# Kernel optimization log

Measured on AMD Instinct MI355X. Metric: run time of the kernel, lower is better.

The kernel has to match this reference:

```python
import jax, jax.numpy as jnp
import numpy as np

M_B, M_S, D_IN, D_OUT = 4, 2048, 4096, 4096
SPARSITY_KEEP = 0.1


def setup_inputs() -> dict:
    key = jax.random.key(0)
    k1, k2, k3, k4 = jax.random.split(key, 4)
    data = jax.random.normal(k1, (M_B, M_S, D_IN), dtype=jnp.float32)
    weight = jax.random.normal(k2, (D_OUT, D_IN), dtype=jnp.float32) * 0.02
    w_mask = (jax.random.uniform(k3, (D_OUT, D_IN)) < SPARSITY_KEEP).astype(jnp.float32)
    bias_p = jax.random.normal(k4, (D_OUT,), dtype=jnp.float32) * 0.02
    return {"data": data, "weight": weight, "w_mask": w_mask, "bias_p": bias_p}


def reference(data, weight, w_mask, bias_p):
    # Equivalent math to CSR-conversion + sparse GEMM: out = data @ (W*mask)^T + b
    w = weight * w_mask                      # [D_OUT, D_IN]
    out = jnp.einsum('bsk,nk->bsn', data, w)  # [B, S, D_OUT]
    return out + bias_p
```

## Files before the change

### kernel.cpp

```cpp
#include <hip/hip_runtime.h>
#include <hip/hip_bf16.h>


#define M_TOT 8192
#define N_TOT 4096
#define K_TOT 4096

#define BM 256
#define BN 256
#define BK 64
#define NT (K_TOT / BK)

typedef __attribute__((ext_vector_type(8))) short short8;
typedef __attribute__((ext_vector_type(4))) float floatx4;

__device__ inline unsigned short f2bf(float f) {
    unsigned int u = __builtin_bit_cast(unsigned int, f);
    u += 0x7fffu + ((u >> 16) & 1u);
    return (unsigned short)(u >> 16);
}

__global__ __launch_bounds__(256) void cast_data_kernel(const float4* __restrict__ in,
                                                        ushort4* __restrict__ out) {
    int i = blockIdx.x * 256 + threadIdx.x;
    float4 f = in[i];
    ushort4 o;
    o.x = f2bf(f.x); o.y = f2bf(f.y); o.z = f2bf(f.z); o.w = f2bf(f.w);
    out[i] = o;
}

__global__ __launch_bounds__(256) void cast_w_kernel(const float4* __restrict__ w,
                                                     const float4* __restrict__ m,
                                                     ushort4* __restrict__ out) {
    int i = blockIdx.x * 256 + threadIdx.x;
    float4 a = w[i];
    float4 b = m[i];
    ushort4 o;
    o.x = f2bf(a.x * b.x); o.y = f2bf(a.y * b.y);
    o.z = f2bf(a.z * b.z); o.w = f2bf(a.w * b.w);
    out[i] = o;
}

__device__ inline void load_lds16(const unsigned short* g, unsigned short* l) {
    __builtin_amdgcn_global_load_lds(
        (__attribute__((address_space(1))) void*)(const_cast<unsigned short*>(g)),
        (__attribute__((address_space(3))) void*)(l),
        16, 0, 0);
}

#define BAR()   __builtin_amdgcn_s_barrier()
#define SB0()   __builtin_amdgcn_sched_barrier(0)
#define LGKM0() do { asm volatile("s_waitcnt lgkmcnt(0)" ::: "memory"); SB0(); } while (0)
#define VM8()   asm volatile("s_waitcnt vmcnt(8)" ::: "memory")
#define VM0()   asm volatile("s_waitcnt vmcnt(0)" ::: "memory")

__global__ __launch_bounds__(512, 2) void gemm_bt_kernel(const unsigned short* __restrict__ A,
                                                         const unsigned short* __restrict__ W,
                                                         const float* __restrict__ bias,
                                                         float* __restrict__ out) {
    __shared__ __align__(16) unsigned short As[2 * BM * BK];
    __shared__ __align__(16) unsigned short Bs[2 * BN * BK];

    const int t = threadIdx.x;
    const int m0 = blockIdx.y * BM;
    const int n0 = blockIdx.x * BN;

    const int lane  = t & 63;
    const int wv    = t >> 6;
    const int wm    = (wv >> 2) * 128;
    const int wn    = (wv & 3) * 64;
    const int row16 = lane & 15;
    const int quad  = lane >> 4;
    const int rx    = row16 & 7;

    const int srow  = t >> 3;
    const int lslot = (t & 7) ^ (srow & 7);
    const size_t thr_off = (size_t)srow * K_TOT + (size_t)lslot * 8;

    const unsigned short* Ag = A + (size_t)m0 * K_TOT + thr_off;
    const unsigned short* Bg = W + (size_t)n0 * K_TOT + thr_off;

    auto stageA = [&](int ts, int h) {
        const unsigned short* s = Ag + (size_t)(h * 128) * K_TOT + ts * BK;
        unsigned short* d = As + (ts & 1) * (BM * BK) + h * (128 * BK) + t * 8;
        load_lds16(s, d);
        load_lds16(s + (size_t)64 * K_TOT, d + 512 * 8);
    };
    auto stageB = [&](int ts, int h) {
        const unsigned short* s = Bg + (size_t)(h * 128) * K_TOT + ts * BK;
        unsigned short* d = Bs + (ts & 1) * (BN * BK) + h * (128 * BK) + t * 8;
        load_lds16(s, d);
        load_lds16(s + (size_t)64 * K_TOT, d + 512 * 8);
    };

    short8 af[4][2];
    short8 bf[2][2][2];

    auto readA_half = [&](int buf, int mh) {
#pragma unroll
        for (int i = 0; i < 4; i++) {
            const unsigned short* base =
                As + buf * (BM * BK) + (wm + mh * 64 + i * 16 + row16) * BK;
            af[i][0] = *(const short8*)(base + ((quad ^ rx) << 3));
            af[i][1] = *(const short8*)(base + (((4 + quad) ^ rx) << 3));
        }
    };
    auto readB_all = [&](int buf) {
#pragma unroll
        for (int nh = 0; nh < 2; nh++)
#pragma unroll
            for (int j = 0; j < 2; j++) {
                const unsigned short* base =
                    Bs + buf * (BN * BK) + (wn + nh * 32 + j * 16 + row16) * BK;
                bf[nh][j][0] = *(const short8*)(base + ((quad ^ rx) << 3));
                bf[nh][j][1] = *(const short8*)(base + (((4 + quad) ^ rx) << 3));
            }
    };

    floatx4 acc[8][4];
#pragma unroll
    for (int i = 0; i < 8; i++)
#pragma unroll
        for (int j = 0; j < 4; j++) {
            floatx4 z = {0.0f, 0.0f, 0.0f, 0.0f};
            acc[i][j] = z;
        }

    auto mmaQ = [&](int mh, int nh) {
        __builtin_amdgcn_s_setprio(1);
#pragma unroll
        for (int i = 0; i < 4; i++)
#pragma unroll
            for (int j = 0; j < 2; j++)
#pragma unroll
                for (int ks = 0; ks < 2; ks++)
                    acc[mh * 4 + i][nh * 2 + j] = __builtin_amdgcn_mfma_f32_16x16x32_bf16(
                        af[i][ks], bf[nh][j][ks], acc[mh * 4 + i][nh * 2 + j], 0, 0, 0);
        __builtin_amdgcn_s_setprio(0);
    };

    auto tile = [&](int kt, int mode) {
        const int buf = kt & 1;
        readA_half(buf, 0);
        readB_all(buf);
        BAR(); LGKM0();
        mmaQ(0, 0);
        BAR();
        if (mode == 0) stageB(kt + 2, 0);
        BAR(); SB0();
        mmaQ(0, 1);
        BAR();
        readA_half(buf, 1);
        if (mode == 0) stageB(kt + 2, 1);
        BAR(); LGKM0();
        mmaQ(1, 1);
        BAR();
        if (mode == 0) { stageA(kt + 2, 0); stageA(kt + 2, 1); VM8(); }
        if (mode == 1) { VM0(); }
        BAR(); SB0();
        mmaQ(1, 0);
        if (mode != 2) BAR();
    };

    stageB(0, 0); stageB(0, 1); stageA(0, 0); stageA(0, 1);
    stageB(1, 0); stageB(1, 1); stageA(1, 0); stageA(1, 1);
    VM8();
    BAR();

    for (int kt = 0; kt < NT - 2; ++kt)
        tile(kt, 0);
    tile(NT - 2, 1);
    tile(NT - 1, 2);

    float bb[4];
#pragma unroll
    for (int j = 0; j < 4; j++)
        bb[j] = bias[n0 + wn + j * 16 + row16];

#pragma unroll
    for (int ai = 0; ai < 8; ai++) {
        const int gm = m0 + wm + ai * 16 + quad * 4;
#pragma unroll
        for (int bj = 0; bj < 4; bj++) {
            const int gn = n0 + wn + bj * 16 + row16;
            float* o = out + (size_t)gm * N_TOT + gn;
#pragma unroll
            for (int r = 0; r < 4; r++)
                o[(size_t)r * N_TOT] = acc[ai][bj][r] + bb[bj];
        }
    }
}

extern "C" void kernel_launch(void* const* d_in, const int* in_sizes, int n_in,
                              void* d_out, int out_size, void* d_ws, size_t ws_size,
                              hipStream_t stream) {
    const float* data   = (const float*)d_in[0];
    const float* weight = (const float*)d_in[1];
    const float* w_mask = (const float*)d_in[2];
    const float* bias_p = (const float*)d_in[3];
    float* out = (float*)d_out;

    unsigned short* a_bf = (unsigned short*)d_ws;
    unsigned short* w_bf = a_bf + (size_t)M_TOT * K_TOT;

    cast_data_kernel<<<(M_TOT * K_TOT) / (256 * 4), 256, 0, stream>>>(
        (const float4*)data, (ushort4*)a_bf);
    cast_w_kernel<<<(N_TOT * K_TOT) / (256 * 4), 256, 0, stream>>>(
        (const float4*)weight, (const float4*)w_mask, (ushort4*)w_bf);

    dim3 grid(N_TOT / BN, M_TOT / BM);
    gemm_bt_kernel<<<grid, 512, 0, stream>>>(a_bf, w_bf, bias_p, out);
}
```

Before: 564.0 us.

## Software-pipeline LDS fragment reads across k-tiles with double-buffered register fragments

```diff
diff --git a/kernel.cpp b/kernel.cpp
--- a/kernel.cpp
+++ b/kernel.cpp
@@ -50,7 +50,6 @@
 
 #define BAR()   __builtin_amdgcn_s_barrier()
 #define SB0()   __builtin_amdgcn_sched_barrier(0)
-#define LGKM0() do { asm volatile("s_waitcnt lgkmcnt(0)" ::: "memory"); SB0(); } while (0)
 #define VM8()   asm volatile("s_waitcnt vmcnt(8)" ::: "memory")
 #define VM0()   asm volatile("s_waitcnt vmcnt(0)" ::: "memory")
 
@@ -93,28 +92,26 @@
         load_lds16(s + (size_t)64 * K_TOT, d + 512 * 8);
     };
 
-    short8 af[4][2];
-    short8 bf[2][2][2];
-
-    auto readA_half = [&](int buf, int mh) {
+    short8 aX[4][2], aY[4][2];
+    short8 b0[2][2], b1[2][2];
+
+    auto readA = [&](int buf, int mh, short8 (&d)[4][2]) {
 #pragma unroll
         for (int i = 0; i < 4; i++) {
             const unsigned short* base =
                 As + buf * (BM * BK) + (wm + mh * 64 + i * 16 + row16) * BK;
-            af[i][0] = *(const short8*)(base + ((quad ^ rx) << 3));
-            af[i][1] = *(const short8*)(base + (((4 + quad) ^ rx) << 3));
-        }
-    };
-    auto readB_all = [&](int buf) {
-#pragma unroll
-        for (int nh = 0; nh < 2; nh++)
-#pragma unroll
-            for (int j = 0; j < 2; j++) {
-                const unsigned short* base =
-                    Bs + buf * (BN * BK) + (wn + nh * 32 + j * 16 + row16) * BK;
-                bf[nh][j][0] = *(const short8*)(base + ((quad ^ rx) << 3));
-                bf[nh][j][1] = *(const short8*)(base + (((4 + quad) ^ rx) << 3));
-            }
+            d[i][0] = *(const short8*)(base + ((quad ^ rx) << 3));
+            d[i][1] = *(const short8*)(base + (((4 + quad) ^ rx) << 3));
+        }
+    };
+    auto readB = [&](int buf, int nh, short8 (&d)[2][2]) {
+#pragma unroll
+        for (int j = 0; j < 2; j++) {
+            const unsigned short* base =
+                Bs + buf * (BN * BK) + (wn + nh * 32 + j * 16 + row16) * BK;
+            d[j][0] = *(const short8*)(base + ((quad ^ rx) << 3));
+            d[j][1] = *(const short8*)(base + (((4 + quad) ^ rx) << 3));
+        }
     };
 
     floatx4 acc[8][4];
@@ -126,7 +123,7 @@
             acc[i][j] = z;
         }
 
-    auto mmaQ = [&](int mh, int nh) {
+    auto mmaQ = [&](short8 (&a)[4][2], short8 (&b)[2][2], int mh, int nh) {
         __builtin_amdgcn_s_setprio(1);
 #pragma unroll
         for (int i = 0; i < 4; i++)
@@ -135,42 +132,46 @@
 #pragma unroll
                 for (int ks = 0; ks < 2; ks++)
                     acc[mh * 4 + i][nh * 2 + j] = __builtin_amdgcn_mfma_f32_16x16x32_bf16(
-                        af[i][ks], bf[nh][j][ks], acc[mh * 4 + i][nh * 2 + j], 0, 0, 0);
+                        a[i][ks], b[j][ks], acc[mh * 4 + i][nh * 2 + j], 0, 0, 0);
         __builtin_amdgcn_s_setprio(0);
     };
 
-    auto tile = [&](int kt, int mode) {
+    auto tileT = [&](int kt, short8 (&aC)[4][2], short8 (&aN)[4][2], int mode) {
         const int buf = kt & 1;
-        readA_half(buf, 0);
-        readB_all(buf);
-        BAR(); LGKM0();
-        mmaQ(0, 0);
-        BAR();
-        if (mode == 0) stageB(kt + 2, 0);
-        BAR(); SB0();
-        mmaQ(0, 1);
-        BAR();
-        readA_half(buf, 1);
-        if (mode == 0) stageB(kt + 2, 1);
-        BAR(); LGKM0();
-        mmaQ(1, 1);
-        BAR();
-        if (mode == 0) { stageA(kt + 2, 0); stageA(kt + 2, 1); VM8(); }
-        if (mode == 1) { VM0(); }
-        BAR(); SB0();
-        mmaQ(1, 0);
-        if (mode != 2) BAR();
-    };
-
-    stageB(0, 0); stageB(0, 1); stageA(0, 0); stageA(0, 1);
-    stageB(1, 0); stageB(1, 1); stageA(1, 0); stageA(1, 1);
+        readA(buf, 1, aN);
+        mmaQ(aC, b0, 0, 0);
+        if (mode != 2) BAR();
+        readB(buf, 1, b1);
+        if (mode == 0) { stageA(kt + 2, 0); stageB(kt + 2, 0); }
+        mmaQ(aN, b0, 1, 0);
+        if (mode != 2) BAR();
+        if (mode == 0) stageA(kt + 2, 1);
+        mmaQ(aN, b1, 1, 1);
+        if (mode != 2) BAR();
+        if (mode == 0) { stageB(kt + 2, 1); VM8(); }
+        else if (mode == 1) { VM0(); }
+        if (mode != 2) {
+            BAR(); SB0();
+            readA(buf ^ 1, 0, aN);
+            readB(buf ^ 1, 0, b0);
+        }
+        mmaQ(aC, b1, 0, 1);
+        if (mode != 2) BAR();
+    };
+
+    stageA(0, 0); stageB(0, 0); stageA(0, 1); stageB(0, 1);
+    stageA(1, 0); stageB(1, 0); stageA(1, 1); stageB(1, 1);
     VM8();
-    BAR();
-
-    for (int kt = 0; kt < NT - 2; ++kt)
-        tile(kt, 0);
-    tile(NT - 2, 1);
-    tile(NT - 1, 2);
+    BAR(); SB0();
+    readA(0, 0, aX);
+    readB(0, 0, b0);
+
+    for (int kt = 0; kt < NT - 2; kt += 2) {
+        tileT(kt,     aX, aY, 0);
+        tileT(kt + 1, aY, aX, 0);
+    }
+    tileT(NT - 2, aX, aY, 1);
+    tileT(NT - 1, aY, aX, 2);
 
     float bb[4];
 #pragma unroll
```

New measurement: 529.9 us. -6.1%, faster.
